# Performance work log

Measured on AMD Instinct MI355X. Metric: run time of the kernel, lower is better.

The kernel has to match this reference:

```python
import jax, jax.numpy as jnp
import numpy as np

B, C, N = 4, 64, 64      # batch, channels (=2*hidden), set size
E = 128                  # set_emb
H = 32                   # hidden_channels


def _unif(k, shape, fan_in):
    lim = 1.0 / np.sqrt(fan_in)
    return jax.random.uniform(k, shape, jnp.float32, -lim, lim)


def setup_inputs() -> dict:
    key = jax.random.key(0)
    ks = jax.random.split(key, 17)
    inp = {"x": jax.random.normal(ks[0], (B, C, N, N), jnp.float32)}
    # set_convs: Linear(4,E) -> ReLU -> Linear(E,E) -> ReLU -> Linear(E,E) -> ReLU -> Linear(E,2)
    inp["W1"] = _unif(ks[1], (4, E), 4);   inp["b1"] = _unif(ks[2], (E,), 4)
    inp["W2"] = _unif(ks[3], (E, E), E);   inp["b2"] = _unif(ks[4], (E,), E)
    inp["W3"] = _unif(ks[5], (E, E), E);   inp["b3"] = _unif(ks[6], (E,), E)
    inp["W4"] = _unif(ks[7], (E, 2), E);   inp["b4"] = _unif(ks[8], (2,), E)
    # channel_fc: 1x1 convs C->128->256->256->H with ReLU between
    inp["Wc1"] = _unif(ks[9], (C, 128), C);     inp["bc1"] = _unif(ks[10], (128,), C)
    inp["Wc2"] = _unif(ks[11], (128, 256), 128); inp["bc2"] = _unif(ks[12], (256,), 128)
    inp["Wc3"] = _unif(ks[13], (256, 256), 256); inp["bc3"] = _unif(ks[14], (256,), 256)
    inp["Wc4"] = _unif(ks[15], (256, H), 256);   inp["bc4"] = _unif(ks[16], (H,), 256)
    return inp


def reference(x, W1, b1, W2, b2, W3, b3, W4, b4,
              Wc1, bc1, Wc2, bc2, Wc3, bc3, Wc4, bc4):
    Bx, Cx, n, _ = x.shape
    # ---- g_x_2to2: gather per-pair 2x2 blocks ----
    d = jnp.diagonal(x, axis1=-2, axis2=-1)              # (B,C,n)
    i = jnp.arange(1, n)[:, None]                        # (n-1,1)
    k = jnp.broadcast_to(jnp.arange(n)[None, :], (n - 1, n))
    j = (k + i) % n                                      # (n-1,n)
    d1 = jnp.broadcast_to(d[:, :, None, :], (Bx, Cx, n - 1, n))  # x[k,k]
    d2 = x[:, :, k, j]                                   # x[k,(k+i)%n]
    d3 = x[:, :, j, k]                                   # x[(k+i)%n,k]
    d4 = d[:, :, j]                                      # x[(k+i)%n,(k+i)%n]
    h = jnp.stack([d1, d2, d3, d4], -1).reshape(Bx, Cx, n * (n - 1), 4)
    # ---- set_convs MLP ----
    h = jax.nn.relu(h @ W1 + b1)
    h = jax.nn.relu(h @ W2 + b2)
    h = jax.nn.relu(h @ W3 + b3)
    h = h @ W4 + b4                                      # (B,C,n(n-1),2)
    # ---- sum_ginv_x_2to2 scatter + coeff ----
    rows = k.reshape(-1)
    cols = j.reshape(-1)
    out = jnp.zeros((Bx, Cx, n, n), x.dtype).at[:, :, rows, cols].set(h[..., 1])
    diag_vals = h[..., 0].reshape(Bx, Cx, n - 1, n).sum(2) / (n - 1)  # coeff diag 1/(n-1)
    out = out + diag_vals[..., :, None] * jnp.eye(n, dtype=x.dtype)
    # ---- channel_fc: 1x1 convs ----
    y = jax.nn.relu(jnp.einsum('bcnm,cd->bdnm', out, Wc1) + bc1[:, None, None])
    y = jax.nn.relu(jnp.einsum('bcnm,cd->bdnm', y, Wc2) + bc2[:, None, None])
    y = jax.nn.relu(jnp.einsum('bcnm,cd->bdnm', y, Wc3) + bc3[:, None, None])
    y = jnp.einsum('bcnm,cd->bdnm', y, Wc4) + bc4[:, None, None]
    return y
```

## Files before the change

### kernel.cpp

```cpp
#include <hip/hip_runtime.h>

typedef __attribute__((ext_vector_type(4))) float f32x4;
typedef __attribute__((ext_vector_type(8))) short s16x8;
typedef __attribute__((ext_vector_type(4))) short s16x4;
typedef __attribute__((ext_vector_type(4))) unsigned u32x4;
typedef __attribute__((ext_vector_type(2))) unsigned u32x2;

__device__ __forceinline__ short f2bf(float f) {
    unsigned u = __builtin_bit_cast(unsigned, f);
    u += 0x7fffu + ((u >> 16) & 1u);
    return (short)(u >> 16);
}
__device__ __forceinline__ unsigned cvt_pk_bf16(float a, float b) {
    unsigned r;
    asm("v_cvt_pk_bf16_f32 %0, %1, %2" : "=v"(r) : "v"(a), "v"(b));
    return r;
}
__device__ __forceinline__ s16x4 pack4(float v0, float v1, float v2, float v3) {
    u32x2 p;
    p[0] = cvt_pk_bf16(v0, v1);
    p[1] = cvt_pk_bf16(v2, v3);
    return __builtin_bit_cast(s16x4, p);
}

__global__ void k_prep(const float* __restrict__ W1,
                       const float* __restrict__ W2, const float* __restrict__ W3,
                       const float* __restrict__ W4,
                       const float* __restrict__ Wc1, const float* __restrict__ Wc2,
                       const float* __restrict__ Wc3, const float* __restrict__ Wc4,
                       short* __restrict__ W1T,
                       short* __restrict__ W2T, short* __restrict__ W3T,
                       float* __restrict__ W4T,
                       short* __restrict__ Wc1T, short* __restrict__ Wc2T,
                       short* __restrict__ Wc3T, short* __restrict__ Wc4T)
{
    int tid = blockIdx.x * 256 + threadIdx.x;
    if (tid < 4096) {
        int n = tid >> 5, k = tid & 31;
        W1T[tid] = (k < 4) ? f2bf(W1[k * 128 + n]) : (short)0;
    }
    if (tid < 16384) {
        int n = tid >> 7, k = tid & 127;
        W2T[tid] = f2bf(W2[k * 128 + n]);
        W3T[tid] = f2bf(W3[k * 128 + n]);
    }
    if (tid < 256) {
        int s = tid >> 7, k = tid & 127;
        W4T[tid] = W4[k * 2 + s];
    }
    if (tid < 8192) {
        int n = tid >> 6, c = tid & 63;
        Wc1T[tid] = f2bf(Wc1[c * 128 + n]);
    }
    if (tid < 32768) {
        int n = tid >> 7, k = tid & 127;
        Wc2T[tid] = f2bf(Wc2[k * 256 + n]);
    }
    if (tid < 65536) {
        int n = tid >> 8, k = tid & 255;
        Wc3T[tid] = f2bf(Wc3[k * 256 + n]);
    }
    if (tid < 8192) {
        int n = tid >> 8, k = tid & 255;
        Wc4T[tid] = f2bf(Wc4[k * 32 + n]);
    }
}

__global__ __launch_bounds__(512, 8)
void k_phase1(const float* __restrict__ x,
              const float* __restrict__ b1, const short* __restrict__ W1T,
              const short* __restrict__ W2T, const float* __restrict__ b2,
              const short* __restrict__ W3T, const float* __restrict__ b3,
              const float* __restrict__ W4T, const float* __restrict__ b4,
              short* __restrict__ outb, float* __restrict__ diagpart)
{
    __shared__ short hA[64 * 128];
    __shared__ float red[8][4][16][2];
    __shared__ float feat[64][4];
    const int t = threadIdx.x;
    const int lane = t & 63;
    const int w = t >> 6;
    const int lr = lane & 15;
    const int hi = lane >> 4;
    const int b = blockIdx.x;
    const int bc = b / 63;
    const int r  = b - bc * 63;
    const int n0 = w * 16;

    if (t < 256) {
        int kk = t & 63, q = t >> 6;
        int jj = (kk + r + 1) & 63;
        const float* xb = x + bc * 4096;
        float v;
        if (q == 0)      v = xb[kk * 65];
        else if (q == 1) v = xb[kk * 64 + jj];
        else if (q == 2) v = xb[jj * 64 + kk];
        else             v = xb[jj * 65];
        feat[kk][q] = v;
    }
    __syncthreads();

    {
        s16x8 aw1 = *(const s16x8*)(W1T + (n0 + lr) * 32 + hi * 8);
        f32x4 acc1[4] = {};
#pragma unroll
        for (int mf = 0; mf < 4; ++mf) {
            u32x4 bw = {0u, 0u, 0u, 0u};
            if (hi == 0) {
                f32x4 fv = *(const f32x4*)(&feat[mf * 16 + lr][0]);
                bw[0] = cvt_pk_bf16(fv[0], fv[1]);
                bw[1] = cvt_pk_bf16(fv[2], fv[3]);
            }
            s16x8 bf = __builtin_bit_cast(s16x8, bw);
            acc1[mf] = __builtin_amdgcn_mfma_f32_16x16x32_bf16(aw1, bf, acc1[mf], 0, 0, 0);
        }
        f32x4 bv = *(const f32x4*)(b1 + n0 + 4 * hi);
#pragma unroll
        for (int mf = 0; mf < 4; ++mf) {
            int m = mf * 16 + lr;
            s16x4 pk = pack4(fmaxf(acc1[mf][0] + bv[0], 0.f),
                             fmaxf(acc1[mf][1] + bv[1], 0.f),
                             fmaxf(acc1[mf][2] + bv[2], 0.f),
                             fmaxf(acc1[mf][3] + bv[3], 0.f));
            int off = (m * 256 + (n0 + 4 * hi) * 2) ^ ((m & 7) << 4);
            *(s16x4*)((char*)hA + off) = pk;
        }
    }
    __syncthreads();

    {
        f32x4 acc[4] = {};
#pragma unroll
        for (int ks = 0; ks < 4; ++ks) {
            const int kb = ks * 32 + hi * 8;
            s16x8 aw = *(const s16x8*)(W2T + (n0 + lr) * 128 + kb);
#pragma unroll
            for (int mf = 0; mf < 4; ++mf) {
                int off = ((mf * 16 + lr) * 256 + kb * 2) ^ ((lr & 7) << 4);
                s16x8 bh = *(const s16x8*)((const char*)hA + off);
                acc[mf] = __builtin_amdgcn_mfma_f32_16x16x32_bf16(aw, bh, acc[mf], 0, 0, 0);
            }
        }
        __syncthreads();
        f32x4 bv = *(const f32x4*)(b2 + n0 + 4 * hi);
#pragma unroll
        for (int mf = 0; mf < 4; ++mf) {
            int m = mf * 16 + lr;
            s16x4 pk = pack4(fmaxf(acc[mf][0] + bv[0], 0.f),
                             fmaxf(acc[mf][1] + bv[1], 0.f),
                             fmaxf(acc[mf][2] + bv[2], 0.f),
                             fmaxf(acc[mf][3] + bv[3], 0.f));
            int off = (m * 256 + (n0 + 4 * hi) * 2) ^ ((m & 7) << 4);
            *(s16x4*)((char*)hA + off) = pk;
        }
    }
    __syncthreads();

    {
        f32x4 acc3[4] = {};
#pragma unroll
        for (int ks = 0; ks < 4; ++ks) {
            const int kb = ks * 32 + hi * 8;
            s16x8 aw = *(const s16x8*)(W3T + (n0 + lr) * 128 + kb);
#pragma unroll
            for (int mf = 0; mf < 4; ++mf) {
                int off = ((mf * 16 + lr) * 256 + kb * 2) ^ ((lr & 7) << 4);
                s16x8 bh = *(const s16x8*)((const char*)hA + off);
                acc3[mf] = __builtin_amdgcn_mfma_f32_16x16x32_bf16(aw, bh, acc3[mf], 0, 0, 0);
            }
        }
        f32x4 bv  = *(const f32x4*)(b3 + n0 + 4 * hi);
        f32x4 w40 = *(const f32x4*)(W4T + n0 + 4 * hi);
        f32x4 w41 = *(const f32x4*)(W4T + 128 + n0 + 4 * hi);
#pragma unroll
        for (int mf = 0; mf < 4; ++mf) {
            float s0 = 0.f, s1 = 0.f;
#pragma unroll
            for (int q = 0; q < 4; ++q) {
                float h = fmaxf(acc3[mf][q] + bv[q], 0.f);
                s0 = fmaf(h, w40[q], s0);
                s1 = fmaf(h, w41[q], s1);
            }
            s0 += __shfl_xor(s0, 16, 64); s0 += __shfl_xor(s0, 32, 64);
            s1 += __shfl_xor(s1, 16, 64); s1 += __shfl_xor(s1, 32, 64);
            if (hi == 0) { red[w][mf][lr][0] = s0; red[w][mf][lr][1] = s1; }
        }
    }
    __syncthreads();
    if (t < 128) {
        int k = t & 63, s = t >> 6;
        int mf = k >> 4, lr2 = k & 15;
        float v = b4[s];
#pragma unroll
        for (int w2 = 0; w2 < 8; ++w2)
            v += red[w2][mf][lr2][s];
        if (s) {
            int jj = (k + r + 1) & 63;
            outb[bc * 4096 + k * 64 + jj] = f2bf(v);
        } else {
            diagpart[b * 64 + k] = v;
        }
    }
}

__global__ void k_diag(const float* __restrict__ diagpart, short* __restrict__ outb)
{
    __shared__ float rds[256];
    const int t = threadIdx.x, bcq = blockIdx.x;
    const int kx = t & 63, q = t >> 6;
    const float* p = diagpart + bcq * 4032 + kx;
    int r0 = q * 16, r1 = (r0 + 16 < 63) ? r0 + 16 : 63;
    float s = 0.f;
    for (int rr = r0; rr < r1; ++rr) s += p[rr * 64];
    rds[t] = s;
    __syncthreads();
    if (t < 64) {
        float v = (rds[t] + rds[t + 64] + rds[t + 128] + rds[t + 192]) * (1.0f / 63.0f);
        outb[bcq * 4096 + t * 65] = f2bf(v);
    }
}

template<int K, int N, bool RELU>
__device__ __forceinline__ void chan_layer16(const short* src, const short* __restrict__ WT,
                                             const float* __restrict__ bias, short* dst,
                                             int w, int lr, int hi)
{
    constexpr int NF = N / 64;
    constexpr int KS = K / 32;
    const int n0 = w * (16 * NF);
    f32x4 acc[NF] = {};
#pragma unroll
    for (int ks = 0; ks < KS; ++ks) {
        const int kb = ks * 32 + hi * 8;
        s16x8 aw[NF];
#pragma unroll
        for (int nf = 0; nf < NF; ++nf)
            aw[nf] = *(const s16x8*)(WT + (n0 + nf * 16 + lr) * K + kb);
        int off = (lr * (K * 2) + kb * 2) ^ ((lr & 7) << 4);
        s16x8 bh = *(const s16x8*)((const char*)src + off);
#pragma unroll
        for (int nf = 0; nf < NF; ++nf)
            acc[nf] = __builtin_amdgcn_mfma_f32_16x16x32_bf16(aw[nf], bh, acc[nf], 0, 0, 0);
    }
#pragma unroll
    for (int nf = 0; nf < NF; ++nf) {
        f32x4 bv = *(const f32x4*)(bias + n0 + nf * 16 + 4 * hi);
        float v0 = acc[nf][0] + bv[0];
        float v1 = acc[nf][1] + bv[1];
        float v2 = acc[nf][2] + bv[2];
        float v3 = acc[nf][3] + bv[3];
        if (RELU) {
            v0 = fmaxf(v0, 0.f); v1 = fmaxf(v1, 0.f);
            v2 = fmaxf(v2, 0.f); v3 = fmaxf(v3, 0.f);
        }
        s16x4 pk = pack4(v0, v1, v2, v3);
        int off = (lr * (N * 2) + (n0 + nf * 16 + 4 * hi) * 2) ^ ((lr & 7) << 4);
        *(s16x4*)((char*)dst + off) = pk;
    }
}

__global__ __launch_bounds__(256, 6)
void k_chanfused(const short* __restrict__ outb,
                 const short* __restrict__ Wc1T, const float* __restrict__ bc1,
                 const short* __restrict__ Wc2T, const float* __restrict__ bc2,
                 const short* __restrict__ Wc3T, const float* __restrict__ bc3,
                 const short* __restrict__ Wc4T, const float* __restrict__ bc4,
                 float* __restrict__ out)
{
    __shared__ short bufA[16 * 256];
    __shared__ short bufB[16 * 256];
    __shared__ float redc[2][16][16];
    const int t = threadIdx.x, lane = t & 63, w = t >> 6;
    const int lr = lane & 15, hi = lane >> 4;
    const int bb = blockIdx.x >> 8;
    const int nm0 = (blockIdx.x & 255) * 16;

    {
        int c = t & 63, rq = t >> 6;
        s16x4 v = *(const s16x4*)(outb + ((size_t)(bb * 64 + c)) * 4096 + nm0 + rq * 4);
#pragma unroll
        for (int q = 0; q < 4; ++q) {
            int row = rq * 4 + q;
            int off = (row * 128 + c * 2) ^ ((row & 7) << 4);
            *(short*)((char*)bufA + off) = v[q];
        }
    }
    __syncthreads();
    chan_layer16< 64, 128, true>(bufA, Wc1T, bc1, bufB, w, lr, hi);
    __syncthreads();
    chan_layer16<128, 256, true>(bufB, Wc2T, bc2, bufA, w, lr, hi);
    __syncthreads();
    chan_layer16<256, 256, true>(bufA, Wc3T, bc3, bufB, w, lr, hi);
    __syncthreads();

    {
        const int wn = w & 1, wk = w >> 1;
        const int n0 = wn * 16;
        f32x4 acc = {};
#pragma unroll
        for (int ks = 0; ks < 4; ++ks) {
            const int kb = (wk * 4 + ks) * 32 + hi * 8;
            s16x8 aw = *(const s16x8*)(Wc4T + (n0 + lr) * 256 + kb);
            int off = (lr * 512 + kb * 2) ^ ((lr & 7) << 4);
            s16x8 bh = *(const s16x8*)((const char*)bufB + off);
            acc = __builtin_amdgcn_mfma_f32_16x16x32_bf16(aw, bh, acc, 0, 0, 0);
        }
        if (wk == 1) {
#pragma unroll
            for (int q = 0; q < 4; ++q)
                redc[wn][4 * hi + q][lr] = acc[q];
        }
        __syncthreads();
        if (wk == 0) {
            f32x4 bv = *(const f32x4*)(bc4 + n0 + 4 * hi);
#pragma unroll
            for (int q = 0; q < 4; ++q) {
                int n = n0 + 4 * hi + q;
                out[((size_t)(bb * 32 + n)) * 4096 + nm0 + lr] =
                    acc[q] + redc[wn][4 * hi + q][lr] + bv[q];
            }
        }
    }
}

extern "C" void kernel_launch(void* const* d_in, const int* in_sizes, int n_in,
                              void* d_out, int out_size, void* d_ws, size_t ws_size,
                              hipStream_t stream)
{
    const float* x   = (const float*)d_in[0];
    const float* W1  = (const float*)d_in[1];
    const float* b1  = (const float*)d_in[2];
    const float* W2  = (const float*)d_in[3];
    const float* b2  = (const float*)d_in[4];
    const float* W3  = (const float*)d_in[5];
    const float* b3  = (const float*)d_in[6];
    const float* W4  = (const float*)d_in[7];
    const float* b4  = (const float*)d_in[8];
    const float* Wc1 = (const float*)d_in[9];
    const float* bc1 = (const float*)d_in[10];
    const float* Wc2 = (const float*)d_in[11];
    const float* bc2 = (const float*)d_in[12];
    const float* Wc3 = (const float*)d_in[13];
    const float* bc3 = (const float*)d_in[14];
    const float* Wc4 = (const float*)d_in[15];
    const float* bc4 = (const float*)d_in[16];
    float* out = (float*)d_out;

    char* ws = (char*)d_ws;
    short* outb     = (short*)(ws);
    float* diagpart = (float*)(ws + (2u << 20));

    size_t off = 8u << 20;
    short* W1T  = (short*)(ws + off); off += 4096 * 2;
    short* W2T  = (short*)(ws + off); off += 16384 * 2;
    short* W3T  = (short*)(ws + off); off += 16384 * 2;
    short* Wc1T = (short*)(ws + off); off += 8192 * 2;
    short* Wc2T = (short*)(ws + off); off += 32768 * 2;
    short* Wc3T = (short*)(ws + off); off += 65536 * 2;
    short* Wc4T = (short*)(ws + off); off += 8192 * 2;
    float* W4T  = (float*)(ws + off); off += 256 * 4;

    k_prep<<<256, 256, 0, stream>>>(W1, W2, W3, W4, Wc1, Wc2, Wc3, Wc4,
                                    W1T, W2T, W3T, W4T, Wc1T, Wc2T, Wc3T, Wc4T);
    k_phase1<<<16128, 512, 0, stream>>>(x, b1, W1T, W2T, b2, W3T, b3, W4T, b4,
                                        outb, diagpart);
    k_diag<<<256, 256, 0, stream>>>(diagpart, outb);
    k_chanfused<<<1024, 256, 0, stream>>>(outb, Wc1T, bc1, Wc2T, bc2,
                                          Wc3T, bc3, Wc4T, bc4, out);
}
```

Measured before the change: 281.3 us.

## Keep set-MLP activations in registers via lane shuffles instead of shared memory

The set-conv MLP kernel is restructured so each wave owns 16 rows and all 128 output features, computing every layer into register accumulators. Between layers the MFMA output fragments are rearranged into B-operand layout with cross-lane shuffles rather than a round trip through an LDS tile. This removes the LDS staging buffer, the reduction buffer and most block barriers, and halves the block to 256 threads. In exchange, each wave reads the full weight matrices from global memory, raising weight traffic per wave, and register pressure goes up.

```diff
diff --git a/kernel.cpp b/kernel.cpp
--- a/kernel.cpp
+++ b/kernel.cpp
@@ -66,7 +66,7 @@
     }
 }
 
-__global__ __launch_bounds__(512, 8)
+__global__ __launch_bounds__(256, 4)
 void k_phase1(const float* __restrict__ x,
               const float* __restrict__ b1, const short* __restrict__ W1T,
               const short* __restrict__ W2T, const float* __restrict__ b2,
@@ -74,8 +74,6 @@
               const float* __restrict__ W4T, const float* __restrict__ b4,
               short* __restrict__ outb, float* __restrict__ diagpart)
 {
-    __shared__ short hA[64 * 128];
-    __shared__ float red[8][4][16][2];
     __shared__ float feat[64][4];
     const int t = threadIdx.x;
     const int lane = t & 63;
@@ -85,9 +83,9 @@
     const int b = blockIdx.x;
     const int bc = b / 63;
     const int r  = b - bc * 63;
-    const int n0 = w * 16;
-
-    if (t < 256) {
+    const int row = w * 16 + lr;
+
+    {
         int kk = t & 63, q = t >> 6;
         int jj = (kk + r + 1) & 63;
         const float* xb = x + bc * 4096;
@@ -100,105 +98,109 @@
     }
     __syncthreads();
 
-    {
-        s16x8 aw1 = *(const s16x8*)(W1T + (n0 + lr) * 32 + hi * 8);
-        f32x4 acc1[4] = {};
-#pragma unroll
-        for (int mf = 0; mf < 4; ++mf) {
-            u32x4 bw = {0u, 0u, 0u, 0u};
-            if (hi == 0) {
-                f32x4 fv = *(const f32x4*)(&feat[mf * 16 + lr][0]);
-                bw[0] = cvt_pk_bf16(fv[0], fv[1]);
-                bw[1] = cvt_pk_bf16(fv[2], fv[3]);
+    f32x4 acc[8];
+    unsigned P[8][2];
+    unsigned Bfr[4][4];
+
+#pragma unroll
+    for (int nt = 0; nt < 8; ++nt)
+        acc[nt] = *(const f32x4*)(b1 + nt * 16 + 4 * hi);
+    {
+        u32x4 bw = {0u, 0u, 0u, 0u};
+        if (hi == 0) {
+            f32x4 fv = *(const f32x4*)(&feat[row][0]);
+            bw[0] = cvt_pk_bf16(fv[0], fv[1]);
+            bw[1] = cvt_pk_bf16(fv[2], fv[3]);
+        }
+        s16x8 bf = __builtin_bit_cast(s16x8, bw);
+#pragma unroll
+        for (int nt = 0; nt < 8; ++nt) {
+            s16x8 aw = *(const s16x8*)(W1T + (nt * 16 + lr) * 32 + hi * 8);
+            acc[nt] = __builtin_amdgcn_mfma_f32_16x16x32_bf16(aw, bf, acc[nt], 0, 0, 0);
+        }
+    }
+#pragma unroll
+    for (int nt = 0; nt < 8; ++nt) {
+        P[nt][0] = cvt_pk_bf16(fmaxf(acc[nt][0], 0.f), fmaxf(acc[nt][1], 0.f));
+        P[nt][1] = cvt_pk_bf16(fmaxf(acc[nt][2], 0.f), fmaxf(acc[nt][3], 0.f));
+    }
+
+#pragma unroll
+    for (int ks = 0; ks < 4; ++ks)
+#pragma unroll
+        for (int j2 = 0; j2 < 2; ++j2) {
+            int src = lr + 16 * (2 * (hi & 1) + j2);
+#pragma unroll
+            for (int h = 0; h < 2; ++h) {
+                unsigned v0 = __shfl((int)P[2 * ks][h],     src, 64);
+                unsigned v1 = __shfl((int)P[2 * ks + 1][h], src, 64);
+                Bfr[ks][j2 * 2 + h] = (hi >> 1) ? v1 : v0;
             }
-            s16x8 bf = __builtin_bit_cast(s16x8, bw);
-            acc1[mf] = __builtin_amdgcn_mfma_f32_16x16x32_bf16(aw1, bf, acc1[mf], 0, 0, 0);
-        }
-        f32x4 bv = *(const f32x4*)(b1 + n0 + 4 * hi);
-#pragma unroll
-        for (int mf = 0; mf < 4; ++mf) {
-            int m = mf * 16 + lr;
-            s16x4 pk = pack4(fmaxf(acc1[mf][0] + bv[0], 0.f),
-                             fmaxf(acc1[mf][1] + bv[1], 0.f),
-                             fmaxf(acc1[mf][2] + bv[2], 0.f),
-                             fmaxf(acc1[mf][3] + bv[3], 0.f));
-            int off = (m * 256 + (n0 + 4 * hi) * 2) ^ ((m & 7) << 4);
-            *(s16x4*)((char*)hA + off) = pk;
-        }
-    }
-    __syncthreads();
-
-    {
-        f32x4 acc[4] = {};
-#pragma unroll
-        for (int ks = 0; ks < 4; ++ks) {
-            const int kb = ks * 32 + hi * 8;
-            s16x8 aw = *(const s16x8*)(W2T + (n0 + lr) * 128 + kb);
-#pragma unroll
-            for (int mf = 0; mf < 4; ++mf) {
-                int off = ((mf * 16 + lr) * 256 + kb * 2) ^ ((lr & 7) << 4);
-                s16x8 bh = *(const s16x8*)((const char*)hA + off);
-                acc[mf] = __builtin_amdgcn_mfma_f32_16x16x32_bf16(aw, bh, acc[mf], 0, 0, 0);
+        }
+
+#pragma unroll
+    for (int nt = 0; nt < 8; ++nt)
+        acc[nt] = *(const f32x4*)(b2 + nt * 16 + 4 * hi);
+#pragma unroll
+    for (int ks = 0; ks < 4; ++ks) {
+        s16x8 bf = __builtin_bit_cast(s16x8, *(const u32x4*)&Bfr[ks][0]);
+#pragma unroll
+        for (int nt = 0; nt < 8; ++nt) {
+            s16x8 aw = *(const s16x8*)(W2T + (nt * 16 + lr) * 128 + ks * 32 + hi * 8);
+            acc[nt] = __builtin_amdgcn_mfma_f32_16x16x32_bf16(aw, bf, acc[nt], 0, 0, 0);
+        }
+    }
+#pragma unroll
+    for (int nt = 0; nt < 8; ++nt) {
+        P[nt][0] = cvt_pk_bf16(fmaxf(acc[nt][0], 0.f), fmaxf(acc[nt][1], 0.f));
+        P[nt][1] = cvt_pk_bf16(fmaxf(acc[nt][2], 0.f), fmaxf(acc[nt][3], 0.f));
+    }
+
+#pragma unroll
+    for (int ks = 0; ks < 4; ++ks)
+#pragma unroll
+        for (int j2 = 0; j2 < 2; ++j2) {
+            int src = lr + 16 * (2 * (hi & 1) + j2);
+#pragma unroll
+            for (int h = 0; h < 2; ++h) {
+                unsigned v0 = __shfl((int)P[2 * ks][h],     src, 64);
+                unsigned v1 = __shfl((int)P[2 * ks + 1][h], src, 64);
+                Bfr[ks][j2 * 2 + h] = (hi >> 1) ? v1 : v0;
             }
         }
-        __syncthreads();
-        f32x4 bv = *(const f32x4*)(b2 + n0 + 4 * hi);
-#pragma unroll
-        for (int mf = 0; mf < 4; ++mf) {
-            int m = mf * 16 + lr;
-            s16x4 pk = pack4(fmaxf(acc[mf][0] + bv[0], 0.f),
-                             fmaxf(acc[mf][1] + bv[1], 0.f),
-                             fmaxf(acc[mf][2] + bv[2], 0.f),
-                             fmaxf(acc[mf][3] + bv[3], 0.f));
-            int off = (m * 256 + (n0 + 4 * hi) * 2) ^ ((m & 7) << 4);
-            *(s16x4*)((char*)hA + off) = pk;
-        }
-    }
-    __syncthreads();
-
-    {
-        f32x4 acc3[4] = {};
-#pragma unroll
-        for (int ks = 0; ks < 4; ++ks) {
-            const int kb = ks * 32 + hi * 8;
-            s16x8 aw = *(const s16x8*)(W3T + (n0 + lr) * 128 + kb);
-#pragma unroll
-            for (int mf = 0; mf < 4; ++mf) {
-                int off = ((mf * 16 + lr) * 256 + kb * 2) ^ ((lr & 7) << 4);
-                s16x8 bh = *(const s16x8*)((const char*)hA + off);
-                acc3[mf] = __builtin_amdgcn_mfma_f32_16x16x32_bf16(aw, bh, acc3[mf], 0, 0, 0);
+
+#pragma unroll
+    for (int nt = 0; nt < 8; ++nt)
+        acc[nt] = *(const f32x4*)(b3 + nt * 16 + 4 * hi);
+#pragma unroll
+    for (int ks = 0; ks < 4; ++ks) {
+        s16x8 bf = __builtin_bit_cast(s16x8, *(const u32x4*)&Bfr[ks][0]);
+#pragma unroll
+        for (int nt = 0; nt < 8; ++nt) {
+            s16x8 aw = *(const s16x8*)(W3T + (nt * 16 + lr) * 128 + ks * 32 + hi * 8);
+            acc[nt] = __builtin_amdgcn_mfma_f32_16x16x32_bf16(aw, bf, acc[nt], 0, 0, 0);
+        }
+    }
+
+    {
+        float s0 = 0.f, s1 = 0.f;
+#pragma unroll
+        for (int nt = 0; nt < 8; ++nt) {
+            f32x4 w40 = *(const f32x4*)(W4T + nt * 16 + 4 * hi);
+            f32x4 w41 = *(const f32x4*)(W4T + 128 + nt * 16 + 4 * hi);
+#pragma unroll
+            for (int q = 0; q < 4; ++q) {
+                float h3 = fmaxf(acc[nt][q], 0.f);
+                s0 = fmaf(h3, w40[q], s0);
+                s1 = fmaf(h3, w41[q], s1);
             }
         }
-        f32x4 bv  = *(const f32x4*)(b3 + n0 + 4 * hi);
-        f32x4 w40 = *(const f32x4*)(W4T + n0 + 4 * hi);
-        f32x4 w41 = *(const f32x4*)(W4T + 128 + n0 + 4 * hi);
-#pragma unroll
-        for (int mf = 0; mf < 4; ++mf) {
-            float s0 = 0.f, s1 = 0.f;
-#pragma unroll
-            for (int q = 0; q < 4; ++q) {
-                float h = fmaxf(acc3[mf][q] + bv[q], 0.f);
-                s0 = fmaf(h, w40[q], s0);
-                s1 = fmaf(h, w41[q], s1);
-            }
-            s0 += __shfl_xor(s0, 16, 64); s0 += __shfl_xor(s0, 32, 64);
-            s1 += __shfl_xor(s1, 16, 64); s1 += __shfl_xor(s1, 32, 64);
-            if (hi == 0) { red[w][mf][lr][0] = s0; red[w][mf][lr][1] = s1; }
-        }
-    }
-    __syncthreads();
-    if (t < 128) {
-        int k = t & 63, s = t >> 6;
-        int mf = k >> 4, lr2 = k & 15;
-        float v = b4[s];
-#pragma unroll
-        for (int w2 = 0; w2 < 8; ++w2)
-            v += red[w2][mf][lr2][s];
-        if (s) {
-            int jj = (k + r + 1) & 63;
-            outb[bc * 4096 + k * 64 + jj] = f2bf(v);
-        } else {
-            diagpart[b * 64 + k] = v;
+        s0 += __shfl_xor(s0, 16, 64); s0 += __shfl_xor(s0, 32, 64);
+        s1 += __shfl_xor(s1, 16, 64); s1 += __shfl_xor(s1, 32, 64);
+        if (hi == 0) {
+            int jj = (row + r + 1) & 63;
+            outb[bc * 4096 + row * 64 + jj] = f2bf(s1 + b4[1]);
+            diagpart[b * 64 + row] = s0 + b4[0];
         }
     }
 }
@@ -362,7 +364,7 @@
 
     k_prep<<<256, 256, 0, stream>>>(W1, W2, W3, W4, Wc1, Wc2, Wc3, Wc4,
                                     W1T, W2T, W3T, W4T, Wc1T, Wc2T, Wc3T, Wc4T);
-    k_phase1<<<16128, 512, 0, stream>>>(x, b1, W1T, W2T, b2, W3T, b3, W4T, b4,
+    k_phase1<<<16128, 256, 0, stream>>>(x, b1, W1T, W2T, b2, W3T, b3, W4T, b4,
                                         outb, diagpart);
     k_diag<<<256, 256, 0, stream>>>(diagpart, outb);
     k_chanfused<<<1024, 256, 0, stream>>>(outb, Wc1T, bc1, Wc2T, bc2,
```

Result: slower. 668.0 us (+137.5%).
